# Performance work log

Hardware: AMD Instinct MI355X
Metric: run time of the kernel (lower is better)

The kernel has to match this reference:

```python
import jax, jax.numpy as jnp
import numpy as np

N_NODES = 100000
N_EDGES = 1600000
D = 128
L = 3
D_OUT = 64


def setup_inputs() -> dict:
    key = jax.random.key(0)
    ks = jax.random.split(key, 6)
    x = jax.random.normal(ks[0], (N_NODES, D), dtype=jnp.float32)
    edge_index = jax.random.randint(ks[1], (2, N_EDGES), 0, N_NODES, dtype=jnp.int64)
    # Kaiming-ish init scale for linear layers
    s = 1.0 / np.sqrt(D)
    W_rel = jax.random.normal(ks[2], (L, D, D), dtype=jnp.float32) * s
    b_rel = jnp.zeros((L, D), dtype=jnp.float32)
    W_root = jax.random.normal(ks[3], (L, D, D), dtype=jnp.float32) * s
    fc_w = jax.random.normal(ks[4], (D_OUT, D), dtype=jnp.float32) * s
    fc_b = jnp.zeros((D_OUT,), dtype=jnp.float32)
    return {"x": x, "edge_index": edge_index, "W_rel": W_rel, "b_rel": b_rel,
            "W_root": W_root, "fc_w": fc_w, "fc_b": fc_b}


def reference(x, edge_index, W_rel, b_rel, W_root, fc_w, fc_b):
    # PyG GraphConv (aggr='add'): x_i' = W_root x_i + W_rel * sum_{j in N(i)} x_j + b
    src, dst = edge_index[0], edge_index[1]
    n = x.shape[0]
    num_layers = W_rel.shape[0]  # static small loop over layers
    for l in range(num_layers):
        agg = jax.ops.segment_sum(x[src], dst, num_segments=n)  # [N, D] scatter-add of gathered neighbor feats
        x = agg @ W_rel[l].T + b_rel[l] + x @ W_root[l].T
    return x @ fc_w.T + fc_b
```

## Files before the change

### kernel.cpp

```cpp
#include <hip/hip_runtime.h>


typedef short bf16x8 __attribute__((ext_vector_type(8)));
typedef float f32x4 __attribute__((ext_vector_type(4)));

#define CAPB 8192

__device__ inline float bf2f(unsigned short u) {
    union { unsigned int i; float f; } v; v.i = ((unsigned int)u) << 16; return v.f;
}
__device__ inline unsigned short f2bf(float f) {
    union { float f; unsigned int i; } v; v.f = f;
    unsigned int r = v.i + 0x7FFFu + ((v.i >> 16) & 1u);
    return (unsigned short)(r >> 16);
}

__global__ __launch_bounds__(512) void prep_kernel(
    const float* __restrict__ Wr2, const float* __restrict__ Wo2,
    const float* __restrict__ fcw, float* __restrict__ K0_2, float* __restrict__ K1_2,
    const int* __restrict__ src, const int* __restrict__ dst,
    int* __restrict__ gcur, unsigned int* __restrict__ bucketed, int e, int NA, int NB) {
    int b = blockIdx.x, t = threadIdx.x;
    if (b < 64) {
        if (t < 256) {
            int matid = b >> 5;
            const float* W = matid ? Wr2 : Wo2;
            float* K = matid ? K1_2 : K0_2;
            int i = t & 127;
            int j = (b & 31) * 2 + (t >> 7);
            float acc = 0.f;
            for (int k = 0; k < 128; k++) acc += W[k * 128 + i] * fcw[j * 128 + k];
            K[i * 64 + j] = acc;
        }
        return;
    }
    b -= 64;
    if (b < NA) {
        __shared__ int sHist[512], sScan[512], sExcl[512], sGbase[512];
        __shared__ unsigned int lbuf[2048];
        __shared__ unsigned short lbkt[2048];
        int e0 = b * 2048;
        int cnt = e - e0; if (cnt > 2048) cnt = 2048;
        sHist[t] = 0;
        __syncthreads();
        unsigned int pk[4]; int bk[4];
#pragma unroll
        for (int k = 0; k < 4; k++) {
            int j = t + k * 512;
            if (j < cnt) {
                int d = dst[e0 + j], s = src[e0 + j];
                bk[k] = d >> 8;
                pk[k] = ((unsigned int)s << 8) | (unsigned int)(d & 255);
                atomicAdd(&sHist[bk[k]], 1);
            } else bk[k] = -1;
        }
        __syncthreads();
        int h = sHist[t];
        if (t < NB && h > 0) sGbase[t] = atomicAdd(&gcur[t], h);
        else sGbase[t] = 0;
        int xv = h; sScan[t] = xv; __syncthreads();
        for (int o = 1; o < 512; o <<= 1) {
            int y = (t >= o) ? sScan[t - o] : 0;
            __syncthreads();
            xv += y; sScan[t] = xv;
            __syncthreads();
        }
        sExcl[t] = xv - h;
        sHist[t] = 0;
        __syncthreads();
#pragma unroll
        for (int k = 0; k < 4; k++) {
            if (bk[k] >= 0) {
                int r = atomicAdd(&sHist[bk[k]], 1);
                int pos = sExcl[bk[k]] + r;
                lbuf[pos] = pk[k];
                lbkt[pos] = (unsigned short)bk[k];
            }
        }
        __syncthreads();
        for (int j = t; j < cnt; j += 512) {
            int b2 = lbkt[j];
            int idx = sGbase[b2] + (j - sExcl[b2]);
            if (idx < CAPB) bucketed[(size_t)b2 * CAPB + idx] = lbuf[j];
        }
    }
}

__global__ __launch_bounds__(256) void partB_kernel(
    const unsigned int* __restrict__ bucketed, const int* __restrict__ gcur,
    int* __restrict__ deg, int* __restrict__ start, int* __restrict__ csr, int n) {
    int b = blockIdx.x, t = threadIdx.x;
    __shared__ int ldeg[256], lscan[256], red[256];
    __shared__ int csr_base_s;
    int cnt = gcur[b]; if (cnt > CAPB) cnt = CAPB;
    int part = 0;
    for (int q = t; q < b; q += 256) { int c = gcur[q]; part += (c > CAPB ? CAPB : c); }
    red[t] = part; __syncthreads();
    for (int o = 128; o > 0; o >>= 1) { if (t < o) red[t] += red[t + o]; __syncthreads(); }
    if (t == 0) csr_base_s = red[0];
    ldeg[t] = 0;
    __syncthreads();
    const unsigned int* bd = bucketed + (size_t)b * CAPB;
    for (int j = t; j < cnt; j += 256) atomicAdd(&ldeg[bd[j] & 255], 1);
    __syncthreads();
    int h = ldeg[t];
    int xv = h; lscan[t] = xv; __syncthreads();
    for (int o = 1; o < 256; o <<= 1) {
        int y = (t >= o) ? lscan[t - o] : 0;
        __syncthreads();
        xv += y; lscan[t] = xv;
        __syncthreads();
    }
    int excl = xv - h;
    int csr_base = csr_base_s;
    int node = b * 256 + t;
    if (node < n) { deg[node] = h; start[node] = csr_base + excl; }
    __syncthreads();
    lscan[t] = excl;
    ldeg[t] = 0;
    __syncthreads();
    for (int j = t; j < cnt; j += 256) {
        unsigned int pkd = bd[j];
        int d = pkd & 255;
        int r = atomicAdd(&ldeg[d], 1);
        csr[csr_base + lscan[d] + r] = (int)(pkd >> 8);
    }
}

__global__ __launch_bounds__(256) void stage2_kernel(
    const float* __restrict__ Wr1, const float* __restrict__ Wo1,
    const float* __restrict__ K0_2, const float* __restrict__ K1_2,
    float* __restrict__ K0_1, float* __restrict__ K1_1, float* __restrict__ K2_1) {
    int b = blockIdx.x, t = threadIdx.x;
    int matid = b >> 5;
    int i = t & 127;
    int j = (b & 31) * 2 + (t >> 7);
    float acc = 0.f;
    if (matid == 0) {
        for (int k = 0; k < 128; k++) acc += Wo1[k * 128 + i] * K0_2[k * 64 + j];
        K0_1[i * 64 + j] = acc;
    } else if (matid == 1) {
        for (int k = 0; k < 128; k++)
            acc += Wr1[k * 128 + i] * K0_2[k * 64 + j] + Wo1[k * 128 + i] * K1_2[k * 64 + j];
        K1_1[i * 64 + j] = acc;
    } else {
        for (int k = 0; k < 128; k++) acc += Wr1[k * 128 + i] * K1_2[k * 64 + j];
        K2_1[i * 64 + j] = acc;
    }
}

__global__ __launch_bounds__(256) void stage3_kernel(
    const float* __restrict__ Wr0, const float* __restrict__ Wo0,
    const float* __restrict__ K0_1, const float* __restrict__ K1_1, const float* __restrict__ K2_1,
    const float* __restrict__ K0_2, const float* __restrict__ K1_2,
    const float* __restrict__ br, const float* __restrict__ fcw, const float* __restrict__ fcb,
    unsigned short* __restrict__ Nw, float* __restrict__ Bv) {
    int b = blockIdx.x, t = threadIdx.x;
    if (b < 128) {
        int matid = b >> 5;
        int i = t & 127;
        int o = (b & 31) * 2 + (t >> 7);
        float acc = 0.f;
        if (matid == 0) {
            for (int k = 0; k < 128; k++) acc += Wo0[k * 128 + i] * K0_1[k * 64 + o];
        } else if (matid == 1) {
            for (int k = 0; k < 128; k++)
                acc += Wr0[k * 128 + i] * K0_1[k * 64 + o] + Wo0[k * 128 + i] * K1_1[k * 64 + o];
        } else if (matid == 2) {
            for (int k = 0; k < 128; k++)
                acc += Wr0[k * 128 + i] * K1_1[k * 64 + o] + Wo0[k * 128 + i] * K2_1[k * 64 + o];
        } else {
            for (int k = 0; k < 128; k++) acc += Wr0[k * 128 + i] * K2_1[k * 64 + o];
        }
        int p = ((o & 3) << 4) | (o >> 2);
        Nw[p * 512 + matid * 128 + i] = f2bf(acc);
        return;
    }
    const float* br0 = br;
    const float* br1 = br + 128;
    const float* br2 = br + 256;
    int j = t & 63;
    int which = t >> 6;
    if (which == 0) {
        float acc = fcb[j];
        for (int k = 0; k < 128; k++) acc += br2[k] * fcw[j * 128 + k];
        for (int k = 0; k < 128; k++) acc += br1[k] * K0_2[k * 64 + j];
        for (int k = 0; k < 128; k++) acc += br0[k] * K0_1[k * 64 + j];
        Bv[j] = acc;
    } else if (which == 1) {
        float acc = 0.f;
        for (int k = 0; k < 128; k++) acc += br1[k] * K1_2[k * 64 + j];
        for (int k = 0; k < 128; k++) acc += br0[k] * K1_1[k * 64 + j];
        Bv[64 + j] = acc;
    } else if (which == 2) {
        float acc = 0.f;
        for (int k = 0; k < 128; k++) acc += br0[k] * K2_1[k * 64 + j];
        Bv[128 + j] = acc;
    }
}

__global__ __launch_bounds__(256, 2) void gemm_u_kernel(
    const float* __restrict__ x, const unsigned short* __restrict__ Nw,
    unsigned short* __restrict__ U, int n) {
    int matid = threadIdx.x >> 6;
    int lane = threadIdx.x & 63;
    int m    = lane & 15;
    int quad = lane >> 4;
    size_t n64 = (size_t)n * 64;
    unsigned short* up = U + (size_t)matid * n64;

    bf16x8 b[4][4];
#pragma unroll
    for (int t = 0; t < 4; t++)
#pragma unroll
        for (int kk = 0; kk < 4; kk++)
            b[t][kk] = *(const bf16x8*)(Nw + (size_t)(t * 16 + m) * 512 + matid * 128 + kk * 32 + quad * 8);

    const int base_tile = blockIdx.x * 8;

    float4 v[8];
    {
        int arow = base_tile * 16 + m; if (arow >= n) arow = n - 1;
        const float* xr = x + (size_t)arow * 128 + quad * 8;
#pragma unroll
        for (int kk = 0; kk < 4; kk++) {
            v[2 * kk]     = *(const float4*)(xr + kk * 32);
            v[2 * kk + 1] = *(const float4*)(xr + kk * 32 + 4);
        }
    }

#pragma unroll
    for (int it = 0; it < 8; it++) {
        int row0 = (base_tile + it) * 16;
        if (row0 >= n) break;

        bf16x8 a[4];
#pragma unroll
        for (int kk = 0; kk < 4; kk++) {
            float4 v0 = v[2 * kk], v1 = v[2 * kk + 1];
            a[kk][0] = (short)f2bf(v0.x); a[kk][1] = (short)f2bf(v0.y);
            a[kk][2] = (short)f2bf(v0.z); a[kk][3] = (short)f2bf(v0.w);
            a[kk][4] = (short)f2bf(v1.x); a[kk][5] = (short)f2bf(v1.y);
            a[kk][6] = (short)f2bf(v1.z); a[kk][7] = (short)f2bf(v1.w);
        }

        if (it < 7 && row0 + 16 < n) {
            int arow = row0 + 16 + m; if (arow >= n) arow = n - 1;
            const float* xr = x + (size_t)arow * 128 + quad * 8;
#pragma unroll
            for (int kk = 0; kk < 4; kk++) {
                v[2 * kk]     = *(const float4*)(xr + kk * 32);
                v[2 * kk + 1] = *(const float4*)(xr + kk * 32 + 4);
            }
        }

        f32x4 acc[4];
#pragma unroll
        for (int t = 0; t < 4; t++) acc[t] = (f32x4){0.f, 0.f, 0.f, 0.f};
#pragma unroll
        for (int kk = 0; kk < 4; kk++)
#pragma unroll
            for (int t = 0; t < 4; t++)
                acc[t] = __builtin_amdgcn_mfma_f32_16x16x32_bf16(a[kk], b[t][kk], acc[t], 0, 0, 0);

#pragma unroll
        for (int r = 0; r < 4; r++) {
            int orow = row0 + quad * 4 + r;
            if (orow < n) {
                ushort4 o4;
                o4.x = f2bf(acc[0][r]); o4.y = f2bf(acc[1][r]);
                o4.z = f2bf(acc[2][r]); o4.w = f2bf(acc[3][r]);
                *(ushort4*)(up + (size_t)orow * 64 + m * 4) = o4;
            }
        }
    }
}

template <int MODE>
__global__ __launch_bounds__(256) void agg64_kernel(
    const unsigned short* __restrict__ in, const unsigned short* __restrict__ addv,
    const int* __restrict__ csr, const int* __restrict__ start, const int* __restrict__ deg,
    unsigned short* __restrict__ outb, float* __restrict__ outf,
    const float* __restrict__ Bv, int* __restrict__ d2w, const int* __restrict__ d2r, int n) {
    int node = blockIdx.x * 4 + (threadIdx.x >> 6);
    if (node >= n) return;
    int lane = threadIdx.x & 63;
    int g  = lane >> 3;
    int fl = lane & 7;

    int s0 = start[node];
    int d  = deg[node];

    float acc[8];
#pragma unroll
    for (int j = 0; j < 8; j++) acc[j] = 0.f;
    int dsum = 0;

#pragma unroll 2
    for (int e0 = 0; e0 < d; e0 += 8) {
        int idx = e0 + g;
        if (idx < d) {
            int s = csr[s0 + idx];
            bf16x8 v = *(const bf16x8*)(in + (size_t)s * 64 + fl * 8);
#pragma unroll
            for (int j = 0; j < 8; j++) acc[j] += bf2f((unsigned short)v[j]);
            if (MODE == 0 && fl == 0) dsum += deg[s];
        }
    }

#pragma unroll
    for (int j = 0; j < 8; j++) {
        acc[j] += __shfl_xor(acc[j], 8);
        acc[j] += __shfl_xor(acc[j], 16);
        acc[j] += __shfl_xor(acc[j], 32);
    }
    if (MODE == 0) {
        dsum += __shfl_xor(dsum, 8);
        dsum += __shfl_xor(dsum, 16);
        dsum += __shfl_xor(dsum, 32);
        if (lane == 0) d2w[node] = dsum;
    }

    if (g == 0) {
        bf16x8 av = *(const bf16x8*)(addv + (size_t)node * 64 + fl * 8);
        if (MODE < 2) {
            bf16x8 o;
#pragma unroll
            for (int j = 0; j < 8; j++) o[j] = (short)f2bf(acc[j] + bf2f((unsigned short)av[j]));
            *(bf16x8*)(outb + (size_t)node * 64 + fl * 8) = o;
        } else {
            float dg = (float)d;
            float dd = (float)d2r[node];
            float ov[8];
#pragma unroll
            for (int j = 0; j < 8; j++) {
                int o = fl * 8 + j;
                ov[j] = acc[j] + bf2f((unsigned short)av[j]) + Bv[o] + dg * Bv[64 + o] + dd * Bv[128 + o];
            }
            float* op = outf + (size_t)node * 64 + fl * 8;
            *(float4*)(op)     = make_float4(ov[0], ov[1], ov[2], ov[3]);
            *(float4*)(op + 4) = make_float4(ov[4], ov[5], ov[6], ov[7]);
        }
    }
}

extern "C" void kernel_launch(void* const* d_in, const int* in_sizes, int n_in,
                              void* d_out, int out_size, void* d_ws, size_t ws_size,
                              hipStream_t stream) {
    const float* x      = (const float*)d_in[0];
    const int*   ei     = (const int*)d_in[1];
    const float* W_rel  = (const float*)d_in[2];
    const float* b_rel  = (const float*)d_in[3];
    const float* W_root = (const float*)d_in[4];
    const float* fc_w   = (const float*)d_in[5];
    const float* fc_b   = (const float*)d_in[6];

    const int n = in_sizes[0] / 128;
    const int e = in_sizes[1] / 2;
    const int* src = ei;
    const int* dst = ei + e;

    const int NB  = (n + 255) >> 8;
    const int NA  = (e + 2047) / 2048;
    const int NT  = (n + 15) / 16;
    const int NGB = (NT + 7) / 8;

    char* p = (char*)d_ws;
    auto take = [&](size_t bytes) -> void* {
        void* r = (void*)p;
        p += (bytes + 255) & ~(size_t)255;
        return r;
    };
    unsigned short* U  = (unsigned short*)take((size_t)n * 256 * 2);
    unsigned short* w1 = (unsigned short*)take((size_t)n * 64 * 2);
    unsigned short* w2 = (unsigned short*)take((size_t)n * 64 * 2);
    int* deg    = (int*)take((size_t)n * 4);
    int* start  = (int*)take((size_t)n * 4);
    int* d2     = (int*)take((size_t)n * 4);
    int* csr    = (int*)take((size_t)e * 4);
    unsigned int* bucketed = (unsigned int*)take((size_t)NB * CAPB * 4);
    int* gcur   = (int*)take((size_t)NB * 4);
    float* K0_2 = (float*)take(128 * 64 * 4);
    float* K1_2 = (float*)take(128 * 64 * 4);
    float* K0_1 = (float*)take(128 * 64 * 4);
    float* K1_1 = (float*)take(128 * 64 * 4);
    float* K2_1 = (float*)take(128 * 64 * 4);
    unsigned short* Nw = (unsigned short*)take(64 * 512 * 2);
    float* Bv   = (float*)take(192 * 4);

    size_t n64 = (size_t)n * 64;
    unsigned short* u0 = U;
    unsigned short* u1 = U + n64;
    unsigned short* u2 = U + 2 * n64;
    unsigned short* u3 = U + 3 * n64;

    hipMemsetAsync(gcur, 0, (size_t)NB * 4, stream);
    prep_kernel<<<64 + NA, 512, 0, stream>>>(
        W_rel + 2 * 16384, W_root + 2 * 16384, fc_w, K0_2, K1_2,
        src, dst, gcur, bucketed, e, NA, NB);
    partB_kernel<<<NB, 256, 0, stream>>>(bucketed, gcur, deg, start, csr, n);
    stage2_kernel<<<96, 256, 0, stream>>>(
        W_rel + 16384, W_root + 16384, K0_2, K1_2, K0_1, K1_1, K2_1);
    stage3_kernel<<<129, 256, 0, stream>>>(
        W_rel, W_root, K0_1, K1_1, K2_1, K0_2, K1_2, b_rel, fc_w, fc_b, Nw, Bv);

    gemm_u_kernel<<<NGB, 256, 0, stream>>>(x, Nw, U, n);

    agg64_kernel<0><<<(n + 3) / 4, 256, 0, stream>>>(
        u3, u2, csr, start, deg, w1, nullptr, nullptr, d2, nullptr, n);
    agg64_kernel<1><<<(n + 3) / 4, 256, 0, stream>>>(
        w1, u1, csr, start, deg, w2, nullptr, nullptr, nullptr, nullptr, n);
    agg64_kernel<2><<<(n + 3) / 4, 256, 0, stream>>>(
        w2, u0, csr, start, deg, nullptr, (float*)d_out, Bv, nullptr, d2, n);
}
```

Before: 366.6 us.

## Map one node per 8 lanes in aggregation kernels, drop cross-lane reduction

The aggregation kernels previously gave each node a full 64-lane wavefront, with 8 edge groups of 8 lanes each followed by shuffle reductions. Now each node gets 8 lanes that walk its neighbor list sequentially, so 32 nodes share a block and no shuffle reduction is needed. This targets wasted lanes and reduction overhead at an average degree of about 16, and gives more independent gathers per wavefront. The cost is a longer serial dependency chain per node and more load imbalance between nodes of different degree within a wavefront. Bias values are also loaded before the loop in the final mode.

```diff
diff --git a/kernel.cpp b/kernel.cpp
--- a/kernel.cpp
+++ b/kernel.cpp
@@ -282,11 +282,19 @@
     const int* __restrict__ csr, const int* __restrict__ start, const int* __restrict__ deg,
     unsigned short* __restrict__ outb, float* __restrict__ outf,
     const float* __restrict__ Bv, int* __restrict__ d2w, const int* __restrict__ d2r, int n) {
-    int node = blockIdx.x * 4 + (threadIdx.x >> 6);
+    int tid = threadIdx.x;
+    int fl  = tid & 7;
+    int node = blockIdx.x * 32 + (tid >> 3);
     if (node >= n) return;
-    int lane = threadIdx.x & 63;
-    int g  = lane >> 3;
-    int fl = lane & 7;
+
+    float b0[8], b1[8], b2[8];
+    if (MODE == 2) {
+#pragma unroll
+        for (int j = 0; j < 8; j++) {
+            int o = fl * 8 + j;
+            b0[j] = Bv[o]; b1[j] = Bv[64 + o]; b2[j] = Bv[128 + o];
+        }
+    }
 
     int s0 = start[node];
     int d  = deg[node];
@@ -296,51 +304,32 @@
     for (int j = 0; j < 8; j++) acc[j] = 0.f;
     int dsum = 0;
 
-#pragma unroll 2
-    for (int e0 = 0; e0 < d; e0 += 8) {
-        int idx = e0 + g;
-        if (idx < d) {
-            int s = csr[s0 + idx];
-            bf16x8 v = *(const bf16x8*)(in + (size_t)s * 64 + fl * 8);
-#pragma unroll
-            for (int j = 0; j < 8; j++) acc[j] += bf2f((unsigned short)v[j]);
-            if (MODE == 0 && fl == 0) dsum += deg[s];
-        }
-    }
-
-#pragma unroll
-    for (int j = 0; j < 8; j++) {
-        acc[j] += __shfl_xor(acc[j], 8);
-        acc[j] += __shfl_xor(acc[j], 16);
-        acc[j] += __shfl_xor(acc[j], 32);
-    }
-    if (MODE == 0) {
-        dsum += __shfl_xor(dsum, 8);
-        dsum += __shfl_xor(dsum, 16);
-        dsum += __shfl_xor(dsum, 32);
-        if (lane == 0) d2w[node] = dsum;
-    }
-
-    if (g == 0) {
-        bf16x8 av = *(const bf16x8*)(addv + (size_t)node * 64 + fl * 8);
-        if (MODE < 2) {
-            bf16x8 o;
-#pragma unroll
-            for (int j = 0; j < 8; j++) o[j] = (short)f2bf(acc[j] + bf2f((unsigned short)av[j]));
-            *(bf16x8*)(outb + (size_t)node * 64 + fl * 8) = o;
-        } else {
-            float dg = (float)d;
-            float dd = (float)d2r[node];
-            float ov[8];
-#pragma unroll
-            for (int j = 0; j < 8; j++) {
-                int o = fl * 8 + j;
-                ov[j] = acc[j] + bf2f((unsigned short)av[j]) + Bv[o] + dg * Bv[64 + o] + dd * Bv[128 + o];
-            }
-            float* op = outf + (size_t)node * 64 + fl * 8;
-            *(float4*)(op)     = make_float4(ov[0], ov[1], ov[2], ov[3]);
-            *(float4*)(op + 4) = make_float4(ov[4], ov[5], ov[6], ov[7]);
-        }
+#pragma unroll 4
+    for (int i = 0; i < d; i++) {
+        int s = csr[s0 + i];
+        bf16x8 v = *(const bf16x8*)(in + (size_t)s * 64 + fl * 8);
+#pragma unroll
+        for (int j = 0; j < 8; j++) acc[j] += bf2f((unsigned short)v[j]);
+        if (MODE == 0 && fl == 0) dsum += deg[s];
+    }
+    if (MODE == 0 && fl == 0) d2w[node] = dsum;
+
+    bf16x8 av = *(const bf16x8*)(addv + (size_t)node * 64 + fl * 8);
+    if (MODE < 2) {
+        bf16x8 o;
+#pragma unroll
+        for (int j = 0; j < 8; j++) o[j] = (short)f2bf(acc[j] + bf2f((unsigned short)av[j]));
+        *(bf16x8*)(outb + (size_t)node * 64 + fl * 8) = o;
+    } else {
+        float dg = (float)d;
+        float dd = (float)d2r[node];
+        float ov[8];
+#pragma unroll
+        for (int j = 0; j < 8; j++)
+            ov[j] = acc[j] + bf2f((unsigned short)av[j]) + b0[j] + dg * b1[j] + dd * b2[j];
+        float* op = outf + (size_t)node * 64 + fl * 8;
+        *(float4*)(op)     = make_float4(ov[0], ov[1], ov[2], ov[3]);
+        *(float4*)(op + 4) = make_float4(ov[4], ov[5], ov[6], ov[7]);
     }
 }
 
@@ -406,10 +395,11 @@
 
     gemm_u_kernel<<<NGB, 256, 0, stream>>>(x, Nw, U, n);
 
-    agg64_kernel<0><<<(n + 3) / 4, 256, 0, stream>>>(
+    const int AGB = (n + 31) / 32;
+    agg64_kernel<0><<<AGB, 256, 0, stream>>>(
         u3, u2, csr, start, deg, w1, nullptr, nullptr, d2, nullptr, n);
-    agg64_kernel<1><<<(n + 3) / 4, 256, 0, stream>>>(
+    agg64_kernel<1><<<AGB, 256, 0, stream>>>(
         w1, u1, csr, start, deg, w2, nullptr, nullptr, nullptr, nullptr, n);
-    agg64_kernel<2><<<(n + 3) / 4, 256, 0, stream>>>(
+    agg64_kernel<2><<<AGB, 256, 0, stream>>>(
         w2, u0, csr, start, deg, nullptr, (float*)d_out, Bv, nullptr, d2, n);
 }
```

Measured after the change: 319.3 us. 1.15x faster.
